# Kernel optimization log

Hardware: AMD Instinct MI355X
Metric: run time of the kernel (lower is better)

## Reference

```python
import jax, jax.numpy as jnp
import numpy as np

B, T, E, H, L, Q, FF, V, C = 4, 2048, 16, 4, 2, 16, 64, 32000, 16
D = E // H  # head_dim = 4


def pos_encoding(t, e):
    # Sinusoidal PE, matching torch: pe[:,0::2]=sin, pe[:,1::2]=cos
    pos = jnp.arange(t, dtype=jnp.float32)[:, None]
    div = jnp.exp(jnp.arange(0, e, 2, dtype=jnp.float32) * (-np.log(10000.0) / e))
    ang = pos * div  # [T, E/2]
    return jnp.stack([jnp.sin(ang), jnp.cos(ang)], axis=-1).reshape(t, e)


def setup_inputs() -> dict:
    key = jax.random.key(0)
    ks = jax.random.split(key, 12)
    def n(k, shape, scale=0.1):
        return (jax.random.normal(k, shape) * scale).astype(jnp.float32)
    return {
        "tokens": jax.random.randint(ks[0], (B, T), 0, V),
        "emb": n(ks[1], (V, E)),
        "Wq": n(ks[2], (L, E, E)), "Wk": n(ks[3], (L, E, E)),
        "Wv": n(ks[4], (L, E, E)), "Wo": n(ks[5], (L, E, E)),
        "theta": n(ks[6], (L, Q), 1.0),
        "W1": n(ks[7], (L, E, FF)), "b1": jnp.zeros((L, FF), jnp.float32),
        "W2": n(ks[8], (L, FF, E)), "b2": jnp.zeros((L, E), jnp.float32),
        "gamma": jnp.ones((E,), jnp.float32), "beta": jnp.zeros((E,), jnp.float32),
        "Wc": n(ks[9], (E, C)), "bc": jnp.zeros((C,), jnp.float32),
    }


def reference(tokens, emb, Wq, Wk, Wv, Wo, theta, W1, b1, W2, b2, gamma, beta, Wc, bc):
    x = emb[tokens] + pos_encoding(T, E)[None]  # [B,T,E]
    for l in range(L):  # fixed small layer count
        # --- multi-head self-attention (no mask, eval mode: dropout off) ---
        q = (x @ Wq[l]).reshape(B, T, H, D)
        k = (x @ Wk[l]).reshape(B, T, H, D)
        v = (x @ Wv[l]).reshape(B, T, H, D)
        scores = jnp.einsum('bqhd,bkhd->bhqk', q, k) / np.sqrt(D).astype(np.float32)
        attn = jax.nn.softmax(scores, axis=-1)  # [B,H,T,T]
        o = jnp.einsum('bhqk,bkhd->bqhd', attn, v).reshape(B, T, E) @ Wo[l]
        x = x + o
        # --- quantum feed-forward ---
        # RX(x_w)|0> then RY(theta_w), measure PauliZ per wire. Single-qubit
        # gates on a product state factorize exactly: <Z_w> = cos(theta_w)*cos(x_w)
        q_out = jnp.cos(theta[l]) * jnp.cos(x)  # [B,T,E]
        h = jax.nn.relu(q_out @ W1[l] + b1[l])
        x = x + (h @ W2[l] + b2[l])
    # final LayerNorm
    mu = x.mean(-1, keepdims=True)
    var = ((x - mu) ** 2).mean(-1, keepdims=True)
    x = (x - mu) / jnp.sqrt(var + 1e-5) * gamma + beta
    # mean pool over tokens + classifier
    return x.mean(axis=1) @ Wc + bc  # [B,C]
```

## Files before the change

kernel.cpp:

```cpp
#include <hip/hip_runtime.h>
#include <hip/hip_bf16.h>
#include <math.h>

#define B_ 4
#define T_ 2048
#define E_ 16
#define H_ 4
#define D_ 4
#define L_ 2
#define FF_ 64
#define C_ 16

#define QSCALE 0.7213475204444817f

typedef __hip_bfloat16 bf16;

#if __has_builtin(__builtin_amdgcn_exp2f)
__device__ __forceinline__ float fast_exp2(float x) { return __builtin_amdgcn_exp2f(x); }
#else
__device__ __forceinline__ float fast_exp2(float x) { return exp2f(x); }
#endif

__device__ __forceinline__ bool probe_bf16(const void* gamma) {
  return ((const unsigned*)gamma)[0] == 0x3F803F80u;
}
__device__ __forceinline__ float ldin(const void* p, int i, bool isb) {
  if (isb) {
    unsigned short u = ((const unsigned short*)p)[i];
    union { unsigned x; float f; } c; c.x = ((unsigned)u) << 16;
    return c.f;
  }
  return ((const float*)p)[i];
}
__device__ __forceinline__ void unpack2(unsigned u, float& a, float& b) {
  union { unsigned x; float f; } lo, hi;
  lo.x = u << 16; hi.x = u & 0xffff0000u;
  a = lo.f; b = hi.f;
}

__global__ __launch_bounds__(64) void embed_kernel(
    const int* __restrict__ tokens, const void* __restrict__ emb,
    const void* __restrict__ gamma, float* __restrict__ X) {
  bool isb = probe_bf16(gamma);
  int row = blockIdx.x * 64 + threadIdx.x;
  int t = row & (T_ - 1);
  int tok = tokens[row];
  float r[16];
  if (isb) {
    const unsigned short* eb = (const unsigned short*)emb + (size_t)tok * E_;
    uint4 e0 = ((const uint4*)eb)[0], e1 = ((const uint4*)eb)[1];
    unpack2(e0.x, r[0], r[1]);   unpack2(e0.y, r[2], r[3]);
    unpack2(e0.z, r[4], r[5]);   unpack2(e0.w, r[6], r[7]);
    unpack2(e1.x, r[8], r[9]);   unpack2(e1.y, r[10], r[11]);
    unpack2(e1.z, r[12], r[13]); unpack2(e1.w, r[14], r[15]);
  } else {
    const float* er = (const float*)emb + (size_t)tok * E_;
    #pragma unroll
    for (int i = 0; i < 4; i++) {
      float4 f = ((const float4*)er)[i];
      r[4*i+0] = f.x; r[4*i+1] = f.y; r[4*i+2] = f.z; r[4*i+3] = f.w;
    }
  }
  const float divs[8] = {1.f, 0.31622776601683794f, 0.1f, 0.031622776601683794f,
                         0.01f, 0.0031622776601683794f, 0.001f, 0.00031622776601683794f};
  #pragma unroll
  for (int i = 0; i < 8; i++) {
    float ang = (float)t * divs[i];
    r[2*i]   += sinf(ang);
    r[2*i+1] += cosf(ang);
  }
  float* xr = X + (size_t)row * E_;
  #pragma unroll
  for (int i = 0; i < 4; i++)
    ((float4*)xr)[i] = make_float4(r[4*i], r[4*i+1], r[4*i+2], r[4*i+3]);
}

__global__ __launch_bounds__(64) void qkv_kernel(
    const float* __restrict__ X,
    const void* __restrict__ Wq, const void* __restrict__ Wk, const void* __restrict__ Wv,
    int wofs, const void* __restrict__ gamma,
    float* __restrict__ Qh, float* __restrict__ KV) {
  __shared__ float wq[16][4], wk[16][4], wv[16][4];
  bool isb = probe_bf16(gamma);
  int tid = threadIdx.x;
  int h  = blockIdx.x >> 7;
  int rb = blockIdx.x & 127;
  {
    int e = tid >> 2, d = tid & 3;
    wq[e][d] = ldin(Wq, wofs + e * 16 + h * 4 + d, isb);
    wk[e][d] = ldin(Wk, wofs + e * 16 + h * 4 + d, isb);
    wv[e][d] = ldin(Wv, wofs + e * 16 + h * 4 + d, isb);
  }
  __syncthreads();
  int row = rb * 64 + tid;
  int b = row >> 11, t = row & (T_ - 1);
  const float* xr = X + (size_t)row * E_;
  float x[16];
  #pragma unroll
  for (int i = 0; i < 4; i++) {
    float4 f = ((const float4*)xr)[i];
    x[4*i]=f.x; x[4*i+1]=f.y; x[4*i+2]=f.z; x[4*i+3]=f.w;
  }
  float q[4] = {0,0,0,0}, k[4] = {0,0,0,0}, v[4] = {0,0,0,0};
  #pragma unroll
  for (int e = 0; e < 16; e++) {
    float xv = x[e];
    #pragma unroll
    for (int d = 0; d < 4; d++) {
      q[d] = fmaf(xv, wq[e][d], q[d]);
      k[d] = fmaf(xv, wk[e][d], k[d]);
      v[d] = fmaf(xv, wv[e][d], v[d]);
    }
  }
  size_t bh = (size_t)(b * H_ + h);
  *(float4*)(Qh + (bh * T_ + t) * 4) =
      make_float4(q[0]*QSCALE, q[1]*QSCALE, q[2]*QSCALE, q[3]*QSCALE);
  float* kvp = KV + (bh * T_ + t) * 8;
  *(float4*)(kvp)     = make_float4(k[0], k[1], k[2], k[3]);
  *(float4*)(kvp + 4) = make_float4(v[0], v[1], v[2], v[3]);
}

__global__ __launch_bounds__(1024) void attn_kernel(
    const float* __restrict__ Qh, const float* __restrict__ KV,
    float* __restrict__ Ob) {
  __shared__ float part[16][64][5];
  int blk = blockIdx.x;
  int bh = blk >> 5;
  int qc = blk & 31;
  int tid = threadIdx.x;
  int qi = tid & 63;
  int ks = __builtin_amdgcn_readfirstlane(tid >> 6);
  int t = qc * 64 + qi;
  float4 q = *(const float4*)(Qh + ((size_t)bh * T_ + t) * 4);
  const float4* kv4 = (const float4*)(KV + ((size_t)bh * T_ + ks * (T_/16)) * 8);
  float l = 0.f, ax = 0.f, ay = 0.f, az = 0.f, aw = 0.f;
  #pragma unroll 8
  for (int j = 0; j < T_/16; j++) {
    float4 k4 = kv4[2*j];
    float4 v4 = kv4[2*j+1];
    float s = fmaf(q.x, k4.x, fmaf(q.y, k4.y, fmaf(q.z, k4.z, q.w * k4.w)));
    float p = fast_exp2(s);
    l += p;
    ax = fmaf(p, v4.x, ax); ay = fmaf(p, v4.y, ay);
    az = fmaf(p, v4.z, az); aw = fmaf(p, v4.w, aw);
  }
  part[ks][qi][0] = ax; part[ks][qi][1] = ay;
  part[ks][qi][2] = az; part[ks][qi][3] = aw;
  part[ks][qi][4] = l;
  __syncthreads();
  if (tid < 64) {
    float sx = 0.f, sy = 0.f, sz = 0.f, sw = 0.f, sl = 0.f;
    #pragma unroll
    for (int w = 0; w < 16; w++) {
      sx += part[w][tid][0]; sy += part[w][tid][1];
      sz += part[w][tid][2]; sw += part[w][tid][3];
      sl += part[w][tid][4];
    }
    float inv = 1.f / sl;
    int b = bh >> 2, h = bh & 3;
    *(float4*)(Ob + ((size_t)b * T_ + qc * 64 + tid) * E_ + h * D_) =
        make_float4(sx * inv, sy * inv, sz * inv, sw * inv);
  }
}

__global__ __launch_bounds__(64) void opff_kernel(
    const float* __restrict__ Ob, const void* __restrict__ Wo, int wofs,
    const void* __restrict__ theta, const void* __restrict__ W1, const void* __restrict__ b1,
    const void* __restrict__ W2, const void* __restrict__ b2, int l,
    const void* __restrict__ gamma, float* __restrict__ X) {
  __shared__ float wo[256], w1[E_*FF_], w2[FF_*E_], s1[FF_], s2[E_], ct[E_];
  bool isb = probe_bf16(gamma);
  int tid = threadIdx.x;
  int o1 = l * E_ * FF_;
  #pragma unroll
  for (int i = tid; i < 256; i += 64) wo[i] = ldin(Wo, wofs + i, isb);
  #pragma unroll
  for (int i = tid; i < E_*FF_; i += 64) {
    w1[i] = ldin(W1, o1 + i, isb);
    w2[i] = ldin(W2, o1 + i, isb);
  }
  if (tid < FF_) s1[tid] = ldin(b1, l*FF_ + tid, isb);
  if (tid < E_) {
    s2[tid] = ldin(b2, l*E_ + tid, isb);
    ct[tid] = cosf(ldin(theta, l*E_ + tid, isb));
  }
  __syncthreads();
  int r = tid & 31;
  int half = tid >> 5;
  size_t row = (size_t)blockIdx.x * 32 + r;
  float* xr = X + row * E_;
  const float* orow = Ob + row * E_;
  float x[16], o[16];
  #pragma unroll
  for (int i = 0; i < 4; i++) {
    float4 f = ((const float4*)xr)[i];
    x[4*i]=f.x; x[4*i+1]=f.y; x[4*i+2]=f.z; x[4*i+3]=f.w;
    float4 g = ((const float4*)orow)[i];
    o[4*i]=g.x; o[4*i+1]=g.y; o[4*i+2]=g.z; o[4*i+3]=g.w;
  }
  #pragma unroll
  for (int c = 0; c < 16; c++) {
    float s = 0.f;
    #pragma unroll
    for (int e = 0; e < 16; e++) s = fmaf(o[e], wo[e*16 + c], s);
    x[c] += s;
  }
  float qo[16];
  #pragma unroll
  for (int e = 0; e < 16; e++) qo[e] = ct[e] * __cosf(x[e]);
  float acc[16];
  #pragma unroll
  for (int e = 0; e < 16; e++) acc[e] = (half == 0) ? s2[e] : 0.f;
  int j0 = half * 32;
  for (int j = j0; j < j0 + 32; j++) {
    float s = s1[j];
    #pragma unroll
    for (int e = 0; e < 16; e++) s = fmaf(qo[e], w1[e*FF_ + j], s);
    s = fmaxf(s, 0.f);
    #pragma unroll
    for (int e = 0; e < 16; e++) acc[e] = fmaf(s, w2[j*E_ + e], acc[e]);
  }
  #pragma unroll
  for (int e = 0; e < 16; e++) acc[e] += __shfl_xor(acc[e], 32, 64);
  if (half == 0) {
    #pragma unroll
    for (int e = 0; e < 16; e++) x[e] += acc[e];
    #pragma unroll
    for (int i = 0; i < 4; i++)
      ((float4*)xr)[i] = make_float4(x[4*i], x[4*i+1], x[4*i+2], x[4*i+3]);
  }
}

__global__ __launch_bounds__(256) void ln_kernel(
    const float* __restrict__ X, const void* __restrict__ gamma, const void* __restrict__ beta,
    float* __restrict__ partial) {
  __shared__ float wsum[4][16];
  __shared__ float sg[16], sb[16];
  bool isb = probe_bf16(gamma);
  int tid = threadIdx.x;
  if (tid < 16) { sg[tid] = ldin(gamma, tid, isb); sb[tid] = ldin(beta, tid, isb); }
  size_t row = (size_t)blockIdx.x * 256 + tid;
  const float* xr = X + row * E_;
  float x[16];
  #pragma unroll
  for (int i = 0; i < 4; i++) {
    float4 f = ((const float4*)xr)[i];
    x[4*i]=f.x; x[4*i+1]=f.y; x[4*i+2]=f.z; x[4*i+3]=f.w;
  }
  float mu = 0.f;
  #pragma unroll
  for (int e = 0; e < 16; e++) mu += x[e];
  mu *= (1.f/16.f);
  float var = 0.f;
  #pragma unroll
  for (int e = 0; e < 16; e++) { float d = x[e]-mu; var = fmaf(d, d, var); }
  var *= (1.f/16.f);
  float inv = rsqrtf(var + 1e-5f);
  __syncthreads();
  float y[16];
  #pragma unroll
  for (int e = 0; e < 16; e++) y[e] = (x[e]-mu)*inv*sg[e] + sb[e];
  #pragma unroll
  for (int e = 0; e < 16; e++) {
    float s = y[e];
    #pragma unroll
    for (int mlane = 1; mlane < 64; mlane <<= 1) s += __shfl_xor(s, mlane, 64);
    y[e] = s;
  }
  if ((tid & 63) == 0) {
    #pragma unroll
    for (int e = 0; e < 16; e++) wsum[tid >> 6][e] = y[e];
  }
  __syncthreads();
  if (tid < 16) {
    float s = wsum[0][tid] + wsum[1][tid] + wsum[2][tid] + wsum[3][tid];
    partial[blockIdx.x * 16 + tid] = s;
  }
}

__global__ __launch_bounds__(64) void finalize_kernel(
    const float* __restrict__ partial, const void* __restrict__ Wc, const void* __restrict__ bc,
    const void* __restrict__ gamma, float* __restrict__ out) {
  __shared__ float pool[4][16];
  bool isb = probe_bf16(gamma);
  int tid = threadIdx.x;
  int b = tid >> 4;
  int e = tid & 15;
  float s = 0.f;
  #pragma unroll
  for (int ch = 0; ch < 8; ch++) s += partial[(b*8+ch)*16 + e];
  pool[b][e] = s * (1.f / T_);
  __syncthreads();
  int c = tid & 15;
  float a = ldin(bc, c, isb);
  #pragma unroll
  for (int ee = 0; ee < 16; ee++) a = fmaf(pool[b][ee], ldin(Wc, ee*16 + c, isb), a);
  out[tid] = a;
}

extern "C" void kernel_launch(void* const* d_in, const int* in_sizes, int n_in,
                              void* d_out, int out_size, void* d_ws, size_t ws_size,
                              hipStream_t stream) {
  const int*  tokens = (const int*)d_in[0];
  const void* emb    = d_in[1];
  const void* Wq     = d_in[2];
  const void* Wk     = d_in[3];
  const void* Wv     = d_in[4];
  const void* Wo     = d_in[5];
  const void* theta  = d_in[6];
  const void* W1     = d_in[7];
  const void* b1     = d_in[8];
  const void* W2     = d_in[9];
  const void* b2     = d_in[10];
  const void* gamma  = d_in[11];
  const void* beta   = d_in[12];
  const void* Wc     = d_in[13];
  const void* bc     = d_in[14];

  float* ws = (float*)d_ws;
  float* X   = ws;
  float* Qh  = ws + 131072;
  float* KV  = ws + 262144;
  float* Ob  = ws + 524288;
  float* Pb  = ws + 655360;
  float* out = (float*)d_out;

  embed_kernel<<<128, 64, 0, stream>>>(tokens, emb, gamma, X);
  for (int l = 0; l < L_; l++) {
    int wofs = l * E_ * E_;
    qkv_kernel<<<512, 64, 0, stream>>>(X, Wq, Wk, Wv, wofs, gamma, Qh, KV);
    attn_kernel<<<B_*H_*(T_/64), 1024, 0, stream>>>(Qh, KV, Ob);
    opff_kernel<<<256, 64, 0, stream>>>(Ob, Wo, wofs, theta, W1, b1, W2, b2, l,
                                        gamma, X);
  }
  ln_kernel<<<32, 256, 0, stream>>>(X, gamma, beta, Pb);
  finalize_kernel<<<1, 64, 0, stream>>>(Pb, Wc, bc, gamma, out);
}
```

Baseline: 91.46 us.

## Transpose K/V to planar layout and use packed float2 FMAs in attention

The QKV kernel now writes K and V in a component-planar layout (one row of T values per dimension) instead of interleaved per token. The attention loop reads four consecutive keys per component as float4 and does the score and accumulation math with 2-wide vector FMAs, which can map to packed FP32 instructions on CDNA. It also adds a min-blocks hint to the attention launch bounds and switches the positional-encoding sin/cos to fast intrinsics. The intent is to cut VALU instruction count in the attention inner loop. The risks are strided scalar stores in the QKV kernel and a small accuracy loss from __sinf/__cosf at large angles.

```diff
diff --git a/kernel.cpp b/kernel.cpp
--- a/kernel.cpp
+++ b/kernel.cpp
@@ -14,6 +14,7 @@
 #define QSCALE 0.7213475204444817f
 
 typedef __hip_bfloat16 bf16;
+typedef float v2 __attribute__((ext_vector_type(2)));
 
 #if __has_builtin(__builtin_amdgcn_exp2f)
 __device__ __forceinline__ float fast_exp2(float x) { return __builtin_amdgcn_exp2f(x); }
@@ -66,8 +67,8 @@
   #pragma unroll
   for (int i = 0; i < 8; i++) {
     float ang = (float)t * divs[i];
-    r[2*i]   += sinf(ang);
-    r[2*i+1] += cosf(ang);
+    r[2*i]   += __sinf(ang);
+    r[2*i+1] += __cosf(ang);
   }
   float* xr = X + (size_t)row * E_;
   #pragma unroll
@@ -79,7 +80,7 @@
     const float* __restrict__ X,
     const void* __restrict__ Wq, const void* __restrict__ Wk, const void* __restrict__ Wv,
     int wofs, const void* __restrict__ gamma,
-    float* __restrict__ Qh, float* __restrict__ KV) {
+    float* __restrict__ Qh, float* __restrict__ KVT) {
   __shared__ float wq[16][4], wk[16][4], wv[16][4];
   bool isb = probe_bf16(gamma);
   int tid = threadIdx.x;
@@ -115,13 +116,13 @@
   size_t bh = (size_t)(b * H_ + h);
   *(float4*)(Qh + (bh * T_ + t) * 4) =
       make_float4(q[0]*QSCALE, q[1]*QSCALE, q[2]*QSCALE, q[3]*QSCALE);
-  float* kvp = KV + (bh * T_ + t) * 8;
-  *(float4*)(kvp)     = make_float4(k[0], k[1], k[2], k[3]);
-  *(float4*)(kvp + 4) = make_float4(v[0], v[1], v[2], v[3]);
-}
-
-__global__ __launch_bounds__(1024) void attn_kernel(
-    const float* __restrict__ Qh, const float* __restrict__ KV,
+  float* kb = KVT + bh * (8 * T_) + t;
+  kb[0*T_] = k[0]; kb[1*T_] = k[1]; kb[2*T_] = k[2]; kb[3*T_] = k[3];
+  kb[4*T_] = v[0]; kb[5*T_] = v[1]; kb[6*T_] = v[2]; kb[7*T_] = v[3];
+}
+
+__global__ __launch_bounds__(1024, 8) void attn_kernel(
+    const float* __restrict__ Qh, const float* __restrict__ KVT,
     float* __restrict__ Ob) {
   __shared__ float part[16][64][5];
   int blk = blockIdx.x;
@@ -132,21 +133,44 @@
   int ks = __builtin_amdgcn_readfirstlane(tid >> 6);
   int t = qc * 64 + qi;
   float4 q = *(const float4*)(Qh + ((size_t)bh * T_ + t) * 4);
-  const float4* kv4 = (const float4*)(KV + ((size_t)bh * T_ + ks * (T_/16)) * 8);
-  float l = 0.f, ax = 0.f, ay = 0.f, az = 0.f, aw = 0.f;
-  #pragma unroll 8
-  for (int j = 0; j < T_/16; j++) {
-    float4 k4 = kv4[2*j];
-    float4 v4 = kv4[2*j+1];
-    float s = fmaf(q.x, k4.x, fmaf(q.y, k4.y, fmaf(q.z, k4.z, q.w * k4.w)));
-    float p = fast_exp2(s);
-    l += p;
-    ax = fmaf(p, v4.x, ax); ay = fmaf(p, v4.y, ay);
-    az = fmaf(p, v4.z, az); aw = fmaf(p, v4.w, aw);
-  }
-  part[ks][qi][0] = ax; part[ks][qi][1] = ay;
-  part[ks][qi][2] = az; part[ks][qi][3] = aw;
-  part[ks][qi][4] = l;
+  const float* base = KVT + (size_t)bh * (8 * T_) + ks * (T_/16);
+  v2 qx = {q.x, q.x}, qy = {q.y, q.y}, qz = {q.z, q.z}, qw = {q.w, q.w};
+  v2 l2 = {0,0}, o0 = {0,0}, o1 = {0,0}, o2 = {0,0}, o3 = {0,0};
+  #pragma unroll 2
+  for (int j = 0; j < T_/16; j += 4) {
+    float4 k0q = *(const float4*)(base + 0*T_ + j);
+    float4 k1q = *(const float4*)(base + 1*T_ + j);
+    float4 k2q = *(const float4*)(base + 2*T_ + j);
+    float4 k3q = *(const float4*)(base + 3*T_ + j);
+    float4 v0q = *(const float4*)(base + 4*T_ + j);
+    float4 v1q = *(const float4*)(base + 5*T_ + j);
+    float4 v2q = *(const float4*)(base + 6*T_ + j);
+    float4 v3q = *(const float4*)(base + 7*T_ + j);
+    v2 sA = qx * (v2){k0q.x, k0q.y};
+    sA = __builtin_elementwise_fma(qy, (v2){k1q.x, k1q.y}, sA);
+    sA = __builtin_elementwise_fma(qz, (v2){k2q.x, k2q.y}, sA);
+    sA = __builtin_elementwise_fma(qw, (v2){k3q.x, k3q.y}, sA);
+    v2 sB = qx * (v2){k0q.z, k0q.w};
+    sB = __builtin_elementwise_fma(qy, (v2){k1q.z, k1q.w}, sB);
+    sB = __builtin_elementwise_fma(qz, (v2){k2q.z, k2q.w}, sB);
+    sB = __builtin_elementwise_fma(qw, (v2){k3q.z, k3q.w}, sB);
+    v2 pA = { fast_exp2(sA.x), fast_exp2(sA.y) };
+    v2 pB = { fast_exp2(sB.x), fast_exp2(sB.y) };
+    l2 += pA; l2 += pB;
+    o0 = __builtin_elementwise_fma(pA, (v2){v0q.x, v0q.y}, o0);
+    o0 = __builtin_elementwise_fma(pB, (v2){v0q.z, v0q.w}, o0);
+    o1 = __builtin_elementwise_fma(pA, (v2){v1q.x, v1q.y}, o1);
+    o1 = __builtin_elementwise_fma(pB, (v2){v1q.z, v1q.w}, o1);
+    o2 = __builtin_elementwise_fma(pA, (v2){v2q.x, v2q.y}, o2);
+    o2 = __builtin_elementwise_fma(pB, (v2){v2q.z, v2q.w}, o2);
+    o3 = __builtin_elementwise_fma(pA, (v2){v3q.x, v3q.y}, o3);
+    o3 = __builtin_elementwise_fma(pB, (v2){v3q.z, v3q.w}, o3);
+  }
+  part[ks][qi][0] = o0.x + o0.y;
+  part[ks][qi][1] = o1.x + o1.y;
+  part[ks][qi][2] = o2.x + o2.y;
+  part[ks][qi][3] = o3.x + o3.y;
+  part[ks][qi][4] = l2.x + l2.y;
   __syncthreads();
   if (tid < 64) {
     float sx = 0.f, sy = 0.f, sz = 0.f, sw = 0.f, sl = 0.f;
@@ -320,7 +344,7 @@
   float* ws = (float*)d_ws;
   float* X   = ws;
   float* Qh  = ws + 131072;
-  float* KV  = ws + 262144;
+  float* KVT = ws + 262144;
   float* Ob  = ws + 524288;
   float* Pb  = ws + 655360;
   float* out = (float*)d_out;
@@ -328,8 +352,8 @@
   embed_kernel<<<128, 64, 0, stream>>>(tokens, emb, gamma, X);
   for (int l = 0; l < L_; l++) {
     int wofs = l * E_ * E_;
-    qkv_kernel<<<512, 64, 0, stream>>>(X, Wq, Wk, Wv, wofs, gamma, Qh, KV);
-    attn_kernel<<<B_*H_*(T_/64), 1024, 0, stream>>>(Qh, KV, Ob);
+    qkv_kernel<<<512, 64, 0, stream>>>(X, Wq, Wk, Wv, wofs, gamma, Qh, KVT);
+    attn_kernel<<<B_*H_*(T_/64), 1024, 0, stream>>>(Qh, KVT, Ob);
     opff_kernel<<<256, 64, 0, stream>>>(Ob, Wo, wofs, theta, W1, b1, W2, b2, l,
                                         gamma, X);
   }
```

Measured after the change: 97.41 us. 1.07x slower.
